# Performance work log

Measured on AMD Instinct MI355X. Metric: run time of the kernel, lower is better.

Reference implementation:

```python
import jax, jax.numpy as jnp
import numpy as np
import math

N = 16
ZIGZAG = np.array([135, 150, 165, 180, 195, 210, 225, 240, 241, 226, 211, 196, 181, 166, 151, 136, 121, 106, 91, 76, 61, 46, 31, 47, 62, 77, 92, 107, 122, 137, 152, 167, 182, 197, 212, 227, 242, 243, 228, 213, 198, 183, 168, 153, 138, 123, 108, 93, 78, 63, 79, 94, 109, 124, 139, 154, 169, 184, 199, 214, 229, 244, 245, 230, 215, 200, 185, 170, 155, 140, 125, 110, 95, 111, 126, 141, 156, 171, 186, 201, 216, 231, 246, 247, 232, 217, 202, 187, 172, 157, 142, 127, 143, 158, 173, 188, 203, 218, 233, 248, 249, 234, 219, 204, 189, 174, 159, 175, 190, 205, 220, 235, 250, 251, 236, 221, 206, 191, 207, 222, 237, 252, 253, 238, 223, 239, 254, 255], dtype=np.int32)

# DCT basis (harmonics) and normalization matrix, matching the torch helpers
_i = np.arange(N, dtype=np.float32)
HARM = np.cos((2.0 * _i[:, None] + 1.0) * (_i[None, :] * math.pi / (2.0 * N))).astype(np.float32)
_n = np.ones((N, 1), dtype=np.float32); _n[0, 0] = 1.0 / math.sqrt(2.0)
NMAT = (_n @ _n.T).astype(np.float32)
SCALE = 1.0 / math.sqrt(2.0 * N)


def setup_inputs() -> dict:
    key = jax.random.key(0)
    x = jax.random.normal(key, (8, 3, 1024, 1024), dtype=jnp.float32)
    return {"x": x}


def reference(x):
    b, c, h, w = x.shape
    # blockify: [b, c, n_blocks, 16, 16], blocks in row-major spatial order
    blocks = x.reshape(b, c, h // N, N, w // N, N).transpose(0, 1, 2, 4, 3, 5).reshape(b, c, -1, N, N)
    harm = jnp.asarray(HARM)
    nmat = jnp.asarray(NMAT)
    # block DCT: scale * n * (H^T @ block @ H)
    coeff = SCALE * nmat * (jnp.matmul(jnp.matmul(harm.T, blocks), harm))
    # zigzag upper-band gather: [b, c, n_blocks, 128]
    flat = coeff.reshape(b, c, -1, N * N)[..., jnp.asarray(ZIGZAG)]
    # adaptive threshold: zero out coefficients below per-block mean
    mean = jnp.mean(flat, axis=3, keepdims=True)
    sel = jnp.where(flat < mean, jnp.float32(0), flat)
    a = jnp.abs(sel) + 1e-12
    # L2 normalize along coefficient dim (torch F.normalize, eps=1e-12)
    norm = jnp.sqrt(jnp.sum(a * a, axis=3, keepdims=True))
    probs = a / jnp.maximum(norm, 1e-12)
    log_prob = jnp.log2(probs)
    entropy = jnp.mean(-jnp.sum(probs * log_prob, axis=3))
    return entropy
```

## Files before the change

### kernel.cpp

```cpp
#include <hip/hip_runtime.h>
#include <math.h>


constexpr double kPi = 3.14159265358979323846;

constexpr double ccos(double x) {
    while (x > kPi) x -= 2.0 * kPi;
    while (x < -kPi) x += 2.0 * kPi;
    double x2 = x * x;
    double term = 1.0, sum = 1.0;
    for (int k = 1; k <= 24; ++k) {
        term *= -x2 / (double)((2 * k - 1) * (2 * k));
        sum += term;
    }
    return sum;
}

struct DctTables {
    float g1[16][16];
    float g2[16][16];
    constexpr DctTables() : g1{}, g2{} {
        for (int j = 0; j < 16; ++j) {
            for (int f = 0; f < 16; ++f) {
                float colf = (float)((double)f * kPi) / 32.0f;
                float arg = (2.0f * (float)j + 1.0f) * colf;
                float h = (float)ccos((double)arg);
                float n = (f == 0) ? 0.70710678118654752440f : 1.0f;
                g1[j][f] = h * n;
                g2[j][f] = h * n * 0.17677669529663688110f;
            }
        }
    }
};
constexpr DctTables kT;

#define NWG 6144
#define NPART (NWG * 4)

#define WAVE_LDS_FENCE() asm volatile("s_waitcnt lgkmcnt(0)" ::: "memory")

__global__ __launch_bounds__(256, 8) void dct_entropy_kernel(
    const float* __restrict__ x, float* __restrict__ partials) {
    __shared__ float smem[4096];

    const int t = threadIdx.x;
    const int wave = t >> 6;
    const int lane = t & 63;
    const int b = lane >> 4;
    const int il = lane & 15;
    float* R = smem + (wave << 10);

    const int g = blockIdx.x;
    const int bc = g >> 8;
    const int br = (g >> 2) & 63;
    const int cg = g & 3;
    const float* gbase =
        x + ((size_t)bc << 20) + ((size_t)br << 14) + (cg << 8) + (wave << 6);

    float4 v4[4];
    {
        const int r0 = lane >> 4;
        const int ch = lane & 15;
#pragma unroll
        for (int k = 0; k < 4; ++k) {
            v4[k] = *(const float4*)(gbase + (size_t)(4 * k + r0) * 1024 +
                                     ch * 4);
        }
#pragma unroll
        for (int k = 0; k < 4; ++k) {
            const int r = 4 * k + r0;
            *(float4*)(&R[(r << 6) + ((ch ^ r) << 2)]) = v4[k];
        }
    }
    WAVE_LDS_FENCE();

    float xr[16];
#pragma unroll
    for (int tt = 0; tt < 4; ++tt) {
        const int ch = 4 * b + tt;
        float4 ld = *(const float4*)(&R[(il << 6) + ((ch ^ il) << 2)]);
        xr[4 * tt + 0] = ld.x;
        xr[4 * tt + 1] = ld.y;
        xr[4 * tt + 2] = ld.z;
        xr[4 * tt + 3] = ld.w;
    }
    WAVE_LDS_FENCE();

    {
        const int cc = (b << 2) + (il >> 2);
        const int lo = il & 3;
#pragma unroll
        for (int v = 0; v < 16; ++v) {
            float acc = 0.0f;
#pragma unroll
            for (int j = 0; j < 16; ++j) acc = fmaf(xr[j], kT.g1[j][v], acc);
            R[(v << 6) + ((cc ^ v) << 2) + lo] = acc;
        }
    }
    WAVE_LDS_FENCE();

    float ti[16];
#pragma unroll
    for (int tt = 0; tt < 4; ++tt) {
        const int ch = 4 * b + tt;
        float4 ld = *(const float4*)(&R[(il << 6) + ((ch ^ il) << 2)]);
        ti[4 * tt + 0] = ld.x;
        ti[4 * tt + 1] = ld.y;
        ti[4 * tt + 2] = ld.z;
        ti[4 * tt + 3] = ld.w;
    }
    WAVE_LDS_FENCE();

    float c[16];
#pragma unroll
    for (int u = 0; u < 16; ++u) {
        float acc = 0.0f;
#pragma unroll
        for (int i = 0; i < 16; ++i) acc = fmaf(ti[i], kT.g2[i][u], acc);
        c[u] = acc;
    }

    const int v = il;
    const int u_min = (v > 7) ? (16 - v) : (15 - v);

    float s = 0.0f;
#pragma unroll
    for (int u = 0; u < 16; ++u) s += (u >= u_min) ? c[u] : 0.0f;
#pragma unroll
    for (int m = 1; m <= 8; m <<= 1) s += __shfl_xor(s, m);
    const float mean = s * (1.0f / 128.0f);

    float a[16];
    float sq = 0.0f;
#pragma unroll
    for (int u = 0; u < 16; ++u) {
        float au = (c[u] < mean) ? 1e-12f : (fabsf(c[u]) + 1e-12f);
        a[u] = (u >= u_min) ? au : 0.0f;
        sq = fmaf(a[u], a[u], sq);
    }
#pragma unroll
    for (int m = 1; m <= 8; m <<= 1) sq += __shfl_xor(sq, m);
    const float inv = 1.0f / fmaxf(sqrtf(sq), 1e-12f);

    float e = 0.0f;
#pragma unroll
    for (int u = 0; u < 16; ++u) {
        float p = a[u] * inv;
        float term = p * __log2f(p);
        e += (u >= u_min) ? term : 0.0f;
    }
#pragma unroll
    for (int m = 1; m <= 32; m <<= 1) e += __shfl_xor(e, m);
    if (lane == 0) partials[(g << 2) + wave] = e;
}

__global__ __launch_bounds__(1024) void reduce_partials(
    const float* __restrict__ partials, float* __restrict__ out) {
    __shared__ float s[16];
    float v = 0.0f;
    const float4* p4 = (const float4*)partials;
    for (int i = threadIdx.x; i < NPART / 4; i += 1024) {
        float4 f = p4[i];
        v += (f.x + f.y) + (f.z + f.w);
    }
#pragma unroll
    for (int m = 1; m <= 32; m <<= 1) v += __shfl_xor(v, m);
    if ((threadIdx.x & 63) == 0) s[threadIdx.x >> 6] = v;
    __syncthreads();
    if (threadIdx.x < 16) {
        float tot = s[threadIdx.x];
#pragma unroll
        for (int m = 1; m <= 8; m <<= 1) tot += __shfl_xor(tot, m);
        if (threadIdx.x == 0) out[0] = tot * (-1.0f / 98304.0f);
    }
}

extern "C" void kernel_launch(void* const* d_in, const int* in_sizes, int n_in,
                              void* d_out, int out_size, void* d_ws,
                              size_t ws_size, hipStream_t stream) {
    const float* x = (const float*)d_in[0];
    float* out = (float*)d_out;
    float* ws = (float*)d_ws;
    dct_entropy_kernel<<<NWG, 256, 0, stream>>>(x, ws);
    reduce_partials<<<1, 1024, 0, stream>>>(ws, out);
}
```

Before: 145.4 us.

## Compute block DCT with bf16 MFMA instructions instead of scalar FMAs

New measurement: 144.3 us. Within noise of the previous version (-0.8%).

```diff
diff --git a/kernel.cpp b/kernel.cpp
--- a/kernel.cpp
+++ b/kernel.cpp
@@ -1,6 +1,9 @@
 #include <hip/hip_runtime.h>
-#include <math.h>
-
+#include <stdint.h>
+
+
+typedef float f32x4 __attribute__((ext_vector_type(4)));
+typedef short bf16x8 __attribute__((ext_vector_type(8)));
 
 constexpr double kPi = 3.14159265358979323846;
 
@@ -16,39 +19,73 @@
     return sum;
 }
 
-struct DctTables {
-    float g1[16][16];
-    float g2[16][16];
-    constexpr DctTables() : g1{}, g2{} {
-        for (int j = 0; j < 16; ++j) {
-            for (int f = 0; f < 16; ++f) {
-                float colf = (float)((double)f * kPi) / 32.0f;
-                float arg = (2.0f * (float)j + 1.0f) * colf;
-                float h = (float)ccos((double)arg);
-                float n = (f == 0) ? 0.70710678118654752440f : 1.0f;
-                g1[j][f] = h * n;
-                g2[j][f] = h * n * 0.17677669529663688110f;
+constexpr float fharm(int i, int f) {
+    float colf = (float)((double)f * kPi) / 32.0f;
+    float arg = (2.0f * (float)i + 1.0f) * colf;
+    return (float)ccos((double)arg);
+}
+
+constexpr uint16_t f2bf(float f) {
+    unsigned u = __builtin_bit_cast(unsigned, f);
+    return (uint16_t)((u + 0x7fffu + ((u >> 16) & 1u)) >> 16);
+}
+
+struct FragTables {
+    alignas(16) uint32_t blo[64][4];
+    alignas(16) uint32_t bhi[64][4];
+    alignas(16) uint32_t a2[64][4];
+    constexpr FragTables() : blo{}, bhi{}, a2{} {
+        for (int l = 0; l < 64; ++l) {
+            const int n = l & 15;
+            const int q = l >> 4;
+            uint16_t slo[8] = {}, shi[8] = {}, sa[8] = {};
+            for (int s = 0; s < 8; ++s) {
+                const int k = 8 * q + s;
+                if (k < 16) {
+                    float g = fharm(k, n) *
+                              ((n == 0) ? 0.70710678118654752440f : 1.0f);
+                    slo[s] = f2bf(g);
+                    sa[s] = f2bf(g * 0.17677669529663688110f);
+                } else {
+                    float g = fharm(k - 16, n) *
+                              ((n == 0) ? 0.70710678118654752440f : 1.0f);
+                    shi[s] = f2bf(g);
+                }
             }
+            for (int d = 0; d < 4; ++d) {
+                blo[l][d] = (uint32_t)slo[2 * d] | ((uint32_t)slo[2 * d + 1] << 16);
+                bhi[l][d] = (uint32_t)shi[2 * d] | ((uint32_t)shi[2 * d + 1] << 16);
+                a2[l][d] = (uint32_t)sa[2 * d] | ((uint32_t)sa[2 * d + 1] << 16);
+            }
         }
     }
 };
-constexpr DctTables kT;
+__constant__ FragTables kF{};
 
 #define NWG 6144
 #define NPART (NWG * 4)
 
 #define WAVE_LDS_FENCE() asm volatile("s_waitcnt lgkmcnt(0)" ::: "memory")
 
-__global__ __launch_bounds__(256, 8) void dct_entropy_kernel(
+__device__ __forceinline__ uint32_t bfr(float f) {
+    uint32_t u = __float_as_uint(f);
+    return (u + 0x7fffu + ((u >> 16) & 1u)) >> 16;
+}
+__device__ __forceinline__ uint32_t pk2(float a, float b) {
+    return bfr(a) | (bfr(b) << 16);
+}
+
+__global__ __launch_bounds__(256, 4) void dct_entropy_kernel(
     const float* __restrict__ x, float* __restrict__ partials) {
-    __shared__ float smem[4096];
+    __shared__ float smem[4 * 1344];
 
     const int t = threadIdx.x;
     const int wave = t >> 6;
     const int lane = t & 63;
-    const int b = lane >> 4;
-    const int il = lane & 15;
-    float* R = smem + (wave << 10);
+    const int l15 = lane & 15;
+    const int q = lane >> 4;
+    float* R = smem + wave * 1344;
+    uint32_t* Rw = (uint32_t*)R;
 
     const int g = blockIdx.x;
     const int bc = g >> 8;
@@ -57,101 +94,100 @@
     const float* gbase =
         x + ((size_t)bc << 20) + ((size_t)br << 14) + (cg << 8) + (wave << 6);
 
-    float4 v4[4];
-    {
-        const int r0 = lane >> 4;
-        const int ch = lane & 15;
+    const float* rp = gbase + (size_t)l15 * 1024 + 8 * q;
+    float4 lo0 = *(const float4*)(rp);
+    float4 hi0 = *(const float4*)(rp + 4);
+    float4 lo1 = *(const float4*)(rp + 32);
+    float4 hi1 = *(const float4*)(rp + 36);
+
+    const bf16x8 fBlo = __builtin_bit_cast(bf16x8, *(const uint4*)kF.blo[lane]);
+    const bf16x8 fBhi = __builtin_bit_cast(bf16x8, *(const uint4*)kF.bhi[lane]);
+    const bf16x8 fA2 = __builtin_bit_cast(bf16x8, *(const uint4*)kF.a2[lane]);
+
+    uint4 ua0 = {pk2(lo0.x, lo0.y), pk2(lo0.z, lo0.w),
+                 pk2(hi0.x, hi0.y), pk2(hi0.z, hi0.w)};
+    uint4 ua1 = {pk2(lo1.x, lo1.y), pk2(lo1.z, lo1.w),
+                 pk2(hi1.x, hi1.y), pk2(hi1.z, hi1.w)};
+    const bf16x8 fA0 = __builtin_bit_cast(bf16x8, ua0);
+    const bf16x8 fA1 = __builtin_bit_cast(bf16x8, ua1);
+
+    const f32x4 z = {0.0f, 0.0f, 0.0f, 0.0f};
+    f32x4 W0 = __builtin_amdgcn_mfma_f32_16x16x32_bf16(fA0, fBlo, z, 0, 0, 0);
+    f32x4 W1 = __builtin_amdgcn_mfma_f32_16x16x32_bf16(fA0, fBhi, z, 0, 0, 0);
+    f32x4 W2 = __builtin_amdgcn_mfma_f32_16x16x32_bf16(fA1, fBlo, z, 0, 0, 0);
+    f32x4 W3 = __builtin_amdgcn_mfma_f32_16x16x32_bf16(fA1, fBhi, z, 0, 0, 0);
+
+    {
+        const int wi = 12 * l15 + 2 * q;
+        *(uint2*)(&Rw[wi]) = make_uint2(pk2(W0.x, W0.y), pk2(W0.z, W0.w));
+        *(uint2*)(&Rw[192 + wi]) = make_uint2(pk2(W1.x, W1.y), pk2(W1.z, W1.w));
+        *(uint2*)(&Rw[384 + wi]) = make_uint2(pk2(W2.x, W2.y), pk2(W2.z, W2.w));
+        *(uint2*)(&Rw[576 + wi]) = make_uint2(pk2(W3.x, W3.y), pk2(W3.z, W3.w));
+    }
+    WAVE_LDS_FENCE();
+
+    bf16x8 fW[4];
+    {
+        const int ri = 12 * l15 + 4 * (q & 1);
+#pragma unroll
+        for (int b = 0; b < 4; ++b)
+            fW[b] = __builtin_bit_cast(bf16x8, *(const uint4*)(&Rw[192 * b + ri]));
+    }
+    WAVE_LDS_FENCE();
+
+    {
+#pragma unroll
+        for (int b = 0; b < 4; ++b) {
+            f32x4 C = __builtin_amdgcn_mfma_f32_16x16x32_bf16(fA2, fW[b], z, 0, 0, 0);
+            *(f32x4*)(&R[324 * b + 20 * l15 + 4 * q]) = C;
+        }
+    }
+    WAVE_LDS_FENCE();
+
+    {
+        const float* C = &R[324 * q + 20 * l15];
+        float c[16];
 #pragma unroll
         for (int k = 0; k < 4; ++k) {
-            v4[k] = *(const float4*)(gbase + (size_t)(4 * k + r0) * 1024 +
-                                     ch * 4);
-        }
-#pragma unroll
-        for (int k = 0; k < 4; ++k) {
-            const int r = 4 * k + r0;
-            *(float4*)(&R[(r << 6) + ((ch ^ r) << 2)]) = v4[k];
-        }
-    }
-    WAVE_LDS_FENCE();
-
-    float xr[16];
-#pragma unroll
-    for (int tt = 0; tt < 4; ++tt) {
-        const int ch = 4 * b + tt;
-        float4 ld = *(const float4*)(&R[(il << 6) + ((ch ^ il) << 2)]);
-        xr[4 * tt + 0] = ld.x;
-        xr[4 * tt + 1] = ld.y;
-        xr[4 * tt + 2] = ld.z;
-        xr[4 * tt + 3] = ld.w;
-    }
-    WAVE_LDS_FENCE();
-
-    {
-        const int cc = (b << 2) + (il >> 2);
-        const int lo = il & 3;
-#pragma unroll
-        for (int v = 0; v < 16; ++v) {
-            float acc = 0.0f;
-#pragma unroll
-            for (int j = 0; j < 16; ++j) acc = fmaf(xr[j], kT.g1[j][v], acc);
-            R[(v << 6) + ((cc ^ v) << 2) + lo] = acc;
-        }
-    }
-    WAVE_LDS_FENCE();
-
-    float ti[16];
-#pragma unroll
-    for (int tt = 0; tt < 4; ++tt) {
-        const int ch = 4 * b + tt;
-        float4 ld = *(const float4*)(&R[(il << 6) + ((ch ^ il) << 2)]);
-        ti[4 * tt + 0] = ld.x;
-        ti[4 * tt + 1] = ld.y;
-        ti[4 * tt + 2] = ld.z;
-        ti[4 * tt + 3] = ld.w;
-    }
-    WAVE_LDS_FENCE();
-
-    float c[16];
-#pragma unroll
-    for (int u = 0; u < 16; ++u) {
-        float acc = 0.0f;
-#pragma unroll
-        for (int i = 0; i < 16; ++i) acc = fmaf(ti[i], kT.g2[i][u], acc);
-        c[u] = acc;
-    }
-
-    const int v = il;
-    const int u_min = (v > 7) ? (16 - v) : (15 - v);
-
-    float s = 0.0f;
-#pragma unroll
-    for (int u = 0; u < 16; ++u) s += (u >= u_min) ? c[u] : 0.0f;
-#pragma unroll
-    for (int m = 1; m <= 8; m <<= 1) s += __shfl_xor(s, m);
-    const float mean = s * (1.0f / 128.0f);
-
-    float a[16];
-    float sq = 0.0f;
-#pragma unroll
-    for (int u = 0; u < 16; ++u) {
-        float au = (c[u] < mean) ? 1e-12f : (fabsf(c[u]) + 1e-12f);
-        a[u] = (u >= u_min) ? au : 0.0f;
-        sq = fmaf(a[u], a[u], sq);
-    }
-#pragma unroll
-    for (int m = 1; m <= 8; m <<= 1) sq += __shfl_xor(sq, m);
-    const float inv = 1.0f / fmaxf(sqrtf(sq), 1e-12f);
-
-    float e = 0.0f;
-#pragma unroll
-    for (int u = 0; u < 16; ++u) {
-        float p = a[u] * inv;
-        float term = p * __log2f(p);
-        e += (u >= u_min) ? term : 0.0f;
-    }
-#pragma unroll
-    for (int m = 1; m <= 32; m <<= 1) e += __shfl_xor(e, m);
-    if (lane == 0) partials[(g << 2) + wave] = e;
+            float4 f = *(const float4*)(C + 4 * k);
+            c[4 * k + 0] = f.x;
+            c[4 * k + 1] = f.y;
+            c[4 * k + 2] = f.z;
+            c[4 * k + 3] = f.w;
+        }
+        const int v = l15;
+        const int u_min = (v > 7) ? (16 - v) : (15 - v);
+
+        float s = 0.0f;
+#pragma unroll
+        for (int u = 0; u < 16; ++u) s += (u >= u_min) ? c[u] : 0.0f;
+#pragma unroll
+        for (int m = 1; m <= 8; m <<= 1) s += __shfl_xor(s, m);
+        const float mean = s * (1.0f / 128.0f);
+
+        float a[16];
+        float sq = 0.0f;
+#pragma unroll
+        for (int u = 0; u < 16; ++u) {
+            float au = (c[u] < mean) ? 1e-12f : (fabsf(c[u]) + 1e-12f);
+            a[u] = (u >= u_min) ? au : 0.0f;
+            sq = fmaf(a[u], a[u], sq);
+        }
+#pragma unroll
+        for (int m = 1; m <= 8; m <<= 1) sq += __shfl_xor(sq, m);
+        const float inv = 1.0f / fmaxf(sqrtf(sq), 1e-12f);
+
+        float e = 0.0f;
+#pragma unroll
+        for (int u = 0; u < 16; ++u) {
+            float p = a[u] * inv;
+            float term = p * __log2f(p);
+            e += (u >= u_min) ? term : 0.0f;
+        }
+#pragma unroll
+        for (int m = 1; m <= 32; m <<= 1) e += __shfl_xor(e, m);
+        if (lane == 0) partials[(g << 2) + wave] = e;
+    }
 }
 
 __global__ __launch_bounds__(1024) void reduce_partials(
```
